# Kernel tuning notes

Measured on AMD Instinct MI355X. Metric: run time of the kernel, lower is better.

Reference implementation:

```python
import jax, jax.numpy as jnp
import numpy as np

GRID_X, GRID_Y, GRID_Z = 200, 200, 8  # grid_size init kwarg (static)


def setup_inputs() -> dict:
    key = jax.random.key(0)
    k1, k2 = jax.random.split(key)
    B, N, D, H, W, C = 4, 6, 41, 16, 44, 64
    # ego-frame points roughly covering the grid extent [-50,50]x[-50,50]x[-4,4]
    scale = jnp.array([55.0, 55.0, 5.0], dtype=jnp.float32)
    geometry = jax.random.uniform(k1, (B, N, D, H, W, 3), dtype=jnp.float32,
                                  minval=-1.0, maxval=1.0) * scale
    features = jax.random.normal(k2, (B, N, D, H, W, C), dtype=jnp.float32)
    voxel_size = jnp.array([0.5, 0.5, 1.0], dtype=jnp.float32)
    voxel_origin = jnp.array([-50.0, -50.0, -4.0], dtype=jnp.float32)
    return {"geometry": geometry, "features": features,
            "voxel_size": voxel_size, "voxel_origin": voxel_origin}


def reference(geometry, features, voxel_size, voxel_origin):
    B = features.shape[0]
    C = features.shape[-1]
    pts = geometry.reshape(B, -1, 3)          # [B, P, 3]
    feat = features.reshape(B, -1, C)         # [B, P, C]

    # metric -> voxel index
    vi = jnp.floor((pts - voxel_origin) / voxel_size).astype(jnp.int32)  # [B, P, 3]
    x, y, z = vi[..., 0], vi[..., 1], vi[..., 2]
    valid = ((x >= 0) & (x < GRID_X) &
             (y >= 0) & (y < GRID_Y) &
             (z >= 0) & (z < GRID_Z))         # [B, P]

    # linear voxel index (z, x, y) ordering; invalid points scatter zeros to slot 0
    lin = z * (GRID_X * GRID_Y) + x * GRID_Y + y
    lin = jnp.where(valid, lin, 0)
    feat_m = jnp.where(valid[..., None], feat, 0.0)

    num_vox = GRID_Z * GRID_X * GRID_Y

    def pool_one(lin_b, feat_b):
        # scatter-add features into dense voxel grid: [num_vox, C]
        return jax.ops.segment_sum(feat_b, lin_b, num_segments=num_vox)

    vox = jax.vmap(pool_one)(lin, feat_m)                         # [B, num_vox, C]
    vox = vox.reshape(B, GRID_Z, GRID_X, GRID_Y, C)
    # torch.cat over z along channel dim => [B, Z*C, X, Y] with z-major blocks
    bev = jnp.transpose(vox, (0, 1, 4, 2, 3)).reshape(B, GRID_Z * C, GRID_X, GRID_Y)
    return bev
```

## Files before the change

### kernel.cpp

```cpp
#include <hip/hip_runtime.h>
#include <hip/hip_bf16.h>


#define GRID_X 200
#define GRID_Y 200
#define GRID_Z 8
#define NCH 64
#define NB 4
#define PTS_PER_BATCH (6 * 41 * 16 * 44)
#define TOTAL_POINTS (NB * PTS_PER_BATCH)
#define OUT_FLOATS ((long long)NB * GRID_Z * NCH * GRID_X * GRID_Y)

#define YT 4
#define TILE_Y 50
#define NBUCKET (NB * GRID_Z * GRID_X * YT)
#define LDS_STRIDE 51

#define WS_CNT     0
#define WS_STARTS  (NBUCKET)
#define WS_CURSOR  (2 * NBUCKET + 1)
#define WS_SORTED  (3 * NBUCKET + 1)
#define WS_INTS    (3 * NBUCKET + 1 + TOTAL_POINTS)

__device__ __forceinline__ bool point_voxel(const float* __restrict__ geom,
                                            const float* __restrict__ vsz,
                                            const float* __restrict__ vorg,
                                            int i, int& vx, int& vy, int& vz) {
    float px = geom[(size_t)i * 3 + 0];
    float py = geom[(size_t)i * 3 + 1];
    float pz = geom[(size_t)i * 3 + 2];
    vx = (int)floorf((px - vorg[0]) / vsz[0]);
    vy = (int)floorf((py - vorg[1]) / vsz[1]);
    vz = (int)floorf((pz - vorg[2]) / vsz[2]);
    return (vx >= 0 && vx < GRID_X && vy >= 0 && vy < GRID_Y &&
            vz >= 0 && vz < GRID_Z);
}

__device__ __forceinline__ int bucket_of(int b, int vz, int vx, int yt) {
    return ((b * GRID_Z + vz) * GRID_X + vx) * YT + yt;
}

__global__ __launch_bounds__(256) void zero_cnt_kernel(int* __restrict__ cnt) {
    int i = blockIdx.x * 256 + threadIdx.x;
    if (i < NBUCKET) cnt[i] = 0;
}

__global__ __launch_bounds__(256) void hist_kernel(
    const float* __restrict__ geom, const float* __restrict__ vsz,
    const float* __restrict__ vorg, int* __restrict__ cnt) {
    int i = blockIdx.x * 256 + threadIdx.x;
    if (i >= TOTAL_POINTS) return;
    int vx, vy, vz;
    if (!point_voxel(geom, vsz, vorg, i, vx, vy, vz)) return;
    int b = i / PTS_PER_BATCH;
    atomicAdd(&cnt[bucket_of(b, vz, vx, vy / TILE_Y)], 1);
}

__global__ __launch_bounds__(256) void scan_kernel(
    const int* __restrict__ cnt, int* __restrict__ starts, int* __restrict__ cursor) {
    __shared__ int partial[256];
    int t = threadIdx.x;
    const int CHUNK = NBUCKET / 256;
    int base = t * CHUNK;
    int s = 0;
    for (int j = 0; j < CHUNK; ++j) s += cnt[base + j];
    partial[t] = s;
    __syncthreads();
    for (int off = 1; off < 256; off <<= 1) {
        int v = (t >= off) ? partial[t - off] : 0;
        __syncthreads();
        partial[t] += v;
        __syncthreads();
    }
    int run = partial[t] - s;
    for (int j = 0; j < CHUNK; ++j) {
        int c = cnt[base + j];
        starts[base + j] = run;
        cursor[base + j] = run;
        run += c;
    }
    if (t == 255) starts[NBUCKET] = run;
}

__global__ __launch_bounds__(256) void scatter_idx_kernel(
    const float* __restrict__ geom, const float* __restrict__ vsz,
    const float* __restrict__ vorg, int* __restrict__ cursor,
    unsigned* __restrict__ sorted) {
    int i = blockIdx.x * 256 + threadIdx.x;
    if (i >= TOTAL_POINTS) return;
    int vx, vy, vz;
    if (!point_voxel(geom, vsz, vorg, i, vx, vy, vz)) return;
    int b = i / PTS_PER_BATCH;
    int yt = vy / TILE_Y;
    int yl = vy - yt * TILE_Y;
    int pos = atomicAdd(&cursor[bucket_of(b, vz, vx, yt)], 1);
    sorted[pos] = (unsigned)i | ((unsigned)yl << 20);
}

__global__ __launch_bounds__(256) void pool_kernel(
    const float* __restrict__ feat, const unsigned* __restrict__ sorted,
    const int* __restrict__ starts, float* __restrict__ out) {
    __shared__ float acc[NCH * LDS_STRIDE];
    int t = threadIdx.x;
    int bid = blockIdx.x;

    for (int j = t; j < NCH * LDS_STRIDE; j += 256) acc[j] = 0.f;
    __syncthreads();

    int s0 = starts[bid];
    int s1 = starts[bid + 1];
    int w = t >> 6;
    int c = t & 63;

    for (int p = s0 + w; p < s1; p += 4) {
        unsigned pk = (unsigned)__builtin_amdgcn_readfirstlane((int)sorted[p]);
        unsigned idx = pk & 0xFFFFFu;
        unsigned yl = pk >> 20;
        float f = feat[(size_t)idx * NCH + c];
        atomicAdd(&acc[c * LDS_STRIDE + yl], f);
    }
    __syncthreads();

    int yt = bid & 3;
    int x = (bid >> 2) % GRID_X;
    int bz = (bid >> 2) / GRID_X;

    int ly = t & 63;
    if (ly < TILE_Y) {
        for (int k = 0; k < 16; ++k) {
            int cc = w + 4 * k;
            size_t o = (((size_t)bz * NCH + cc) * GRID_X + x) * GRID_Y
                       + (size_t)yt * TILE_Y + ly;
            out[o] = acc[cc * LDS_STRIDE + ly];
        }
    }
}

__global__ __launch_bounds__(256) void zero_out_kernel(float4* __restrict__ out) {
    const long long n4 = OUT_FLOATS / 4;
    long long stride = (long long)gridDim.x * blockDim.x;
    for (long long i = blockIdx.x * (long long)blockDim.x + threadIdx.x;
         i < n4; i += stride)
        out[i] = make_float4(0.f, 0.f, 0.f, 0.f);
}

__global__ __launch_bounds__(256) void voxel_scatter_kernel(
    const float* __restrict__ geom, const float* __restrict__ feat,
    const float* __restrict__ vsz, const float* __restrict__ vorg,
    float* __restrict__ out) {
    int gid = blockIdx.x * blockDim.x + threadIdx.x;
    int pt = gid >> 6;
    int c = gid & 63;
    if (pt >= TOTAL_POINTS) return;
    int vx, vy, vz;
    if (!point_voxel(geom, vsz, vorg, pt, vx, vy, vz)) return;
    int b = pt / PTS_PER_BATCH;
    float f = feat[(size_t)pt * NCH + c];
    size_t idx = ((((size_t)b * GRID_Z + vz) * NCH + c) * GRID_X + vx) * GRID_Y + vy;
    atomicAdd(out + idx, f);
}

extern "C" void kernel_launch(void* const* d_in, const int* in_sizes, int n_in,
                              void* d_out, int out_size, void* d_ws, size_t ws_size,
                              hipStream_t stream) {
    const float* geom = (const float*)d_in[0];
    const float* feat = (const float*)d_in[1];
    const float* vsz  = (const float*)d_in[2];
    const float* vorg = (const float*)d_in[3];
    float* out = (float*)d_out;

    if (ws_size >= (size_t)WS_INTS * sizeof(int)) {
        int* ws = (int*)d_ws;
        int* cnt = ws + WS_CNT;
        int* starts = ws + WS_STARTS;
        int* cursor = ws + WS_CURSOR;
        unsigned* sorted = (unsigned*)(ws + WS_SORTED);

        zero_cnt_kernel<<<(NBUCKET + 255) / 256, 256, 0, stream>>>(cnt);
        hist_kernel<<<TOTAL_POINTS / 256, 256, 0, stream>>>(geom, vsz, vorg, cnt);
        scan_kernel<<<1, 256, 0, stream>>>(cnt, starts, cursor);
        scatter_idx_kernel<<<TOTAL_POINTS / 256, 256, 0, stream>>>(
            geom, vsz, vorg, cursor, sorted);
        pool_kernel<<<NBUCKET, 256, 0, stream>>>(feat, sorted, starts, out);
    } else {
        zero_out_kernel<<<2048, 256, 0, stream>>>((float4*)out);
        const long long total_threads = (long long)TOTAL_POINTS * NCH;
        voxel_scatter_kernel<<<(int)((total_threads + 255) / 256), 256, 0, stream>>>(
            geom, feat, vsz, vorg, out);
    }
}
```

Baseline: 621.8 us.

## Cache per-point bucket codes, widen y-tiles, and vectorize pool gathers and stores

The histogram pass now writes a packed per-point code (valid flag, bucket, local y), so the scatter pass no longer reloads geometry or recomputes voxel indices. Y-tiles grow from 50 to 100, which halves the number of buckets and pool blocks. The pool kernel switches to a y-major LDS layout: 16 lanes gather one point's 64 channels as float4 loads, so one wavefront handles four points per step, and the transposed result is written to the output with float4 stores. The cost is an extra workspace array and strided LDS reads during the transpose, and the 14-bit bucket field must still cover the new bucket count (12800).

Result: faster. 604.1 us (-2.8%).

```diff
diff --git a/kernel.cpp b/kernel.cpp
--- a/kernel.cpp
+++ b/kernel.cpp
@@ -11,16 +11,17 @@
 #define TOTAL_POINTS (NB * PTS_PER_BATCH)
 #define OUT_FLOATS ((long long)NB * GRID_Z * NCH * GRID_X * GRID_Y)
 
-#define YT 4
-#define TILE_Y 50
+#define YT 2
+#define TILE_Y 100
 #define NBUCKET (NB * GRID_Z * GRID_X * YT)
-#define LDS_STRIDE 51
+#define LDS_STRIDE 65
 
 #define WS_CNT     0
 #define WS_STARTS  (NBUCKET)
 #define WS_CURSOR  (2 * NBUCKET + 1)
 #define WS_SORTED  (3 * NBUCKET + 1)
-#define WS_INTS    (3 * NBUCKET + 1 + TOTAL_POINTS)
+#define WS_PCODE   (3 * NBUCKET + 1 + TOTAL_POINTS)
+#define WS_INTS    (3 * NBUCKET + 1 + 2 * TOTAL_POINTS)
 
 __device__ __forceinline__ bool point_voxel(const float* __restrict__ geom,
                                             const float* __restrict__ vsz,
@@ -36,10 +37,6 @@
             vz >= 0 && vz < GRID_Z);
 }
 
-__device__ __forceinline__ int bucket_of(int b, int vz, int vx, int yt) {
-    return ((b * GRID_Z + vz) * GRID_X + vx) * YT + yt;
-}
-
 __global__ __launch_bounds__(256) void zero_cnt_kernel(int* __restrict__ cnt) {
     int i = blockIdx.x * 256 + threadIdx.x;
     if (i < NBUCKET) cnt[i] = 0;
@@ -47,13 +44,21 @@
 
 __global__ __launch_bounds__(256) void hist_kernel(
     const float* __restrict__ geom, const float* __restrict__ vsz,
-    const float* __restrict__ vorg, int* __restrict__ cnt) {
+    const float* __restrict__ vorg, int* __restrict__ cnt,
+    unsigned* __restrict__ pcode) {
     int i = blockIdx.x * 256 + threadIdx.x;
     if (i >= TOTAL_POINTS) return;
     int vx, vy, vz;
-    if (!point_voxel(geom, vsz, vorg, i, vx, vy, vz)) return;
-    int b = i / PTS_PER_BATCH;
-    atomicAdd(&cnt[bucket_of(b, vz, vx, vy / TILE_Y)], 1);
+    unsigned code = 0;
+    if (point_voxel(geom, vsz, vorg, i, vx, vy, vz)) {
+        int b = i / PTS_PER_BATCH;
+        int yt = vy / TILE_Y;
+        int yl = vy - yt * TILE_Y;
+        int bucket = ((b * GRID_Z + vz) * GRID_X + vx) * YT + yt;
+        code = 0x80000000u | ((unsigned)yl << 14) | (unsigned)bucket;
+        atomicAdd(&cnt[bucket], 1);
+    }
+    pcode[i] = code;
 }
 
 __global__ __launch_bounds__(256) void scan_kernel(
@@ -83,56 +88,67 @@
 }
 
 __global__ __launch_bounds__(256) void scatter_idx_kernel(
-    const float* __restrict__ geom, const float* __restrict__ vsz,
-    const float* __restrict__ vorg, int* __restrict__ cursor,
+    const unsigned* __restrict__ pcode, int* __restrict__ cursor,
     unsigned* __restrict__ sorted) {
     int i = blockIdx.x * 256 + threadIdx.x;
     if (i >= TOTAL_POINTS) return;
-    int vx, vy, vz;
-    if (!point_voxel(geom, vsz, vorg, i, vx, vy, vz)) return;
-    int b = i / PTS_PER_BATCH;
-    int yt = vy / TILE_Y;
-    int yl = vy - yt * TILE_Y;
-    int pos = atomicAdd(&cursor[bucket_of(b, vz, vx, yt)], 1);
-    sorted[pos] = (unsigned)i | ((unsigned)yl << 20);
+    unsigned code = pcode[i];
+    if (!(code & 0x80000000u)) return;
+    int bucket = (int)(code & 0x3FFFu);
+    unsigned yl = (code >> 14) & 0x7Fu;
+    int pos = atomicAdd(&cursor[bucket], 1);
+    sorted[pos] = (unsigned)i | (yl << 20);
 }
 
 __global__ __launch_bounds__(256) void pool_kernel(
-    const float* __restrict__ feat, const unsigned* __restrict__ sorted,
-    const int* __restrict__ starts, float* __restrict__ out) {
-    __shared__ float acc[NCH * LDS_STRIDE];
+    const float4* __restrict__ feat4, const unsigned* __restrict__ sorted,
+    const int* __restrict__ starts, float4* __restrict__ out4) {
+    __shared__ __align__(16) float acc[TILE_Y * LDS_STRIDE];
     int t = threadIdx.x;
     int bid = blockIdx.x;
 
-    for (int j = t; j < NCH * LDS_STRIDE; j += 256) acc[j] = 0.f;
+    float4* a4 = (float4*)acc;
+    for (int i = t; i < TILE_Y * LDS_STRIDE / 4; i += 256)
+        a4[i] = make_float4(0.f, 0.f, 0.f, 0.f);
     __syncthreads();
 
     int s0 = starts[bid];
     int s1 = starts[bid + 1];
     int w = t >> 6;
-    int c = t & 63;
-
-    for (int p = s0 + w; p < s1; p += 4) {
-        unsigned pk = (unsigned)__builtin_amdgcn_readfirstlane((int)sorted[p]);
-        unsigned idx = pk & 0xFFFFFu;
-        unsigned yl = pk >> 20;
-        float f = feat[(size_t)idx * NCH + c];
-        atomicAdd(&acc[c * LDS_STRIDE + yl], f);
+    int g = (t >> 4) & 3;
+    int l = t & 15;
+
+    for (int p0 = s0 + w * 4; p0 < s1; p0 += 16) {
+        int p = p0 + g;
+        if (p < s1) {
+            unsigned pk = sorted[p];
+            unsigned idx = pk & 0xFFFFFu;
+            unsigned yl = pk >> 20;
+            float4 f = feat4[(size_t)idx * 16 + l];
+            float* row = &acc[yl * LDS_STRIDE + 4 * l];
+            atomicAdd(row + 0, f.x);
+            atomicAdd(row + 1, f.y);
+            atomicAdd(row + 2, f.z);
+            atomicAdd(row + 3, f.w);
+        }
     }
     __syncthreads();
 
-    int yt = bid & 3;
-    int x = (bid >> 2) % GRID_X;
-    int bz = (bid >> 2) / GRID_X;
-
-    int ly = t & 63;
-    if (ly < TILE_Y) {
-        for (int k = 0; k < 16; ++k) {
-            int cc = w + 4 * k;
-            size_t o = (((size_t)bz * NCH + cc) * GRID_X + x) * GRID_Y
-                       + (size_t)yt * TILE_Y + ly;
-            out[o] = acc[cc * LDS_STRIDE + ly];
-        }
+    int yt = bid & 1;
+    int x = (bid >> 1) % GRID_X;
+    int bz = (bid >> 1) / GRID_X;
+
+    for (int i = t; i < NCH * (TILE_Y / 4); i += 256) {
+        int cc = i / (TILE_Y / 4);
+        int j = i % (TILE_Y / 4);
+        int y0 = 4 * j;
+        float4 v = make_float4(acc[(y0 + 0) * LDS_STRIDE + cc],
+                               acc[(y0 + 1) * LDS_STRIDE + cc],
+                               acc[(y0 + 2) * LDS_STRIDE + cc],
+                               acc[(y0 + 3) * LDS_STRIDE + cc]);
+        size_t o4 = (((size_t)bz * NCH + cc) * GRID_X + x) * (GRID_Y / 4)
+                    + yt * (TILE_Y / 4) + j;
+        out4[o4] = v;
     }
 }
 
@@ -175,13 +191,14 @@
         int* starts = ws + WS_STARTS;
         int* cursor = ws + WS_CURSOR;
         unsigned* sorted = (unsigned*)(ws + WS_SORTED);
+        unsigned* pcode  = (unsigned*)(ws + WS_PCODE);
 
         zero_cnt_kernel<<<(NBUCKET + 255) / 256, 256, 0, stream>>>(cnt);
-        hist_kernel<<<TOTAL_POINTS / 256, 256, 0, stream>>>(geom, vsz, vorg, cnt);
+        hist_kernel<<<TOTAL_POINTS / 256, 256, 0, stream>>>(geom, vsz, vorg, cnt, pcode);
         scan_kernel<<<1, 256, 0, stream>>>(cnt, starts, cursor);
-        scatter_idx_kernel<<<TOTAL_POINTS / 256, 256, 0, stream>>>(
-            geom, vsz, vorg, cursor, sorted);
-        pool_kernel<<<NBUCKET, 256, 0, stream>>>(feat, sorted, starts, out);
+        scatter_idx_kernel<<<TOTAL_POINTS / 256, 256, 0, stream>>>(pcode, cursor, sorted);
+        pool_kernel<<<NBUCKET, 256, 0, stream>>>(
+            (const float4*)feat, sorted, starts, (float4*)out);
     } else {
         zero_out_kernel<<<2048, 256, 0, stream>>>((float4*)out);
         const long long total_threads = (long long)TOTAL_POINTS * NCH;
```
